# Optimization experiments

Hardware: AMD Instinct MI355X
Metric: run time of the kernel (lower is better)

Reference implementation:

```python
import jax, jax.numpy as jnp
import numpy as np

N = 16384
K = 16

def _w(k, shape):
    return jax.random.normal(k, shape, jnp.float32) * 0.05

def setup_inputs() -> dict:
    key = jax.random.key(0)
    ks = jax.random.split(key, 20)
    return {
        "img_feat": jax.random.normal(ks[0], (1, 32, N), jnp.float32),
        "cloud": jax.random.uniform(ks[1], (1, N, 3), jnp.float32),
        "conv1_w": _w(ks[2], (64, 32)),   "conv1_b": _w(ks[3], (64,)),
        "conv2_w": _w(ks[4], (128, 64)),  "conv2_b": _w(ks[5], (128,)),
        "psconv1_w": _w(ks[6], (256, 128)), "psconv1_b": _w(ks[7], (256,)),
        "psconv2_w": _w(ks[8], (128, 256)), "psconv2_b": _w(ks[9], (128,)),
        "pconv1_w": _w(ks[10], (64, 3)),  "pconv1_b": _w(ks[11], (64,)),
        "pconv2_w": _w(ks[12], (128, 64)),"pconv2_b": _w(ks[13], (128,)),
        "final_w": _w(ks[14], (32, 416)), "final_b": _w(ks[15], (32,)),
        "topk": K,
    }

def reference(img_feat, cloud, conv1_w, conv1_b, conv2_w, conv2_b,
              psconv1_w, psconv1_b, psconv2_w, psconv2_b,
              pconv1_w, pconv1_b, pconv2_w, pconv2_b,
              final_w, final_b, topk):
    lrelu = lambda x: jax.nn.leaky_relu(x, 0.01)
    pts = cloud[0]            # [N,3]  (module assumes bs=1)
    imf = img_feat[0].T       # [N,32]
    # point MLP: pconv1 -> lrelu -> pconv2 (Conv1d kernel=1 == per-point linear)
    cf = lrelu(pts @ pconv1_w.T + pconv1_b) @ pconv2_w.T + pconv2_b  # [N,128]
    # KNN: k smallest euclidean distances (self included)
    sq = jnp.sum(pts * pts, axis=-1)                 # [N]
    d2 = sq[:, None] + sq[None, :] - 2.0 * (pts @ pts.T)  # [N,N]
    _, idx = jax.lax.top_k(-d2, topk)                # [N,K]
    nb_pts = pts[idx]                                # [N,K,3]
    dist = jnp.sqrt(jnp.maximum(jnp.sum((pts[:, None, :] - nb_pts) ** 2, -1), 1e-12))
    wgt = jax.nn.softmax(-dist, axis=1)              # [N,K]
    nb_img = imf[idx]                                # [N,K,32]
    nb_cf = cf[idx]                                  # [N,K,128]
    sf = lrelu(nb_img @ conv1_w.T + conv1_b) @ conv2_w.T + conv2_b         # [N,K,128]
    sfp = lrelu(nb_cf @ psconv1_w.T + psconv1_b) @ psconv2_w.T + psconv2_b # [N,K,128]
    sf = jnp.max(sf * wgt[:, :, None], axis=1)       # weighted max-pool -> [N,128]
    sfp = jnp.max(sfp * wgt[:, :, None], axis=1)     # [N,128]
    final = jnp.concatenate([sfp, imf, sf, cf], axis=1)  # [N,416]
    out = lrelu(final) @ final_w.T + final_b         # [N,32]
    return out.T[None]                               # [1,32,N]
```

## Files before the change

### kernel.cpp

```cpp
#include <hip/hip_runtime.h>
#include <math.h>

#define N 16384
#define KNN 16
#define G 14
#define NCELL (G * G * G)

typedef __attribute__((ext_vector_type(8))) short bf16x8;
typedef __attribute__((ext_vector_type(4))) float f32x4;
typedef unsigned short ushort_t;
typedef unsigned long long u64;

__device__ __forceinline__ float lrelu(float a) { return a > 0.f ? a : 0.01f * a; }

__device__ __forceinline__ ushort_t f2bf(float f) {
  unsigned u = __float_as_uint(f);
  u += 0x7FFF + ((u >> 16) & 1);
  return (ushort_t)(u >> 16);
}
__device__ __forceinline__ float bf2f(ushort_t h) {
  return __uint_as_float((unsigned)h << 16);
}
__device__ __forceinline__ int lanerank(u64 mask) {
  return __builtin_amdgcn_mbcnt_hi((unsigned)(mask >> 32),
         __builtin_amdgcn_mbcnt_lo((unsigned)mask, 0));
}
__device__ __forceinline__ int cellof(float x) {
  int c = (int)(x * (float)G);
  return c < 0 ? 0 : (c > G - 1 ? G - 1 : c);
}
__device__ __forceinline__ int cellid(float x, float y, float z) {
  return (cellof(z) * G + cellof(y)) * G + cellof(x);
}

#define PPB 64
__global__ __launch_bounds__(256) void prepw_kernel(
    const float* __restrict__ img, const float* __restrict__ cloud,
    const float* __restrict__ p1w, const float* __restrict__ p1b,
    const float* __restrict__ p2w, const float* __restrict__ p2b,
    const float* __restrict__ ps1w, const float* __restrict__ ps2w,
    const float* __restrict__ c1w, const float* __restrict__ c2w,
    const float* __restrict__ fw,
    float4* __restrict__ pts4, ushort_t* __restrict__ cfh,
    ushort_t* __restrict__ imfh,
    ushort_t* __restrict__ w1h, ushort_t* __restrict__ w2h,
    ushort_t* __restrict__ c1h, ushort_t* __restrict__ c2h,
    float* __restrict__ fwp2, int* __restrict__ count) {
  int t = threadIdx.x;
  if (blockIdx.x >= 256) {
    int e = (blockIdx.x - 256) * 256 + t;
    if (e < 32768) w1h[e] = f2bf(ps1w[e]);
    else if (e < 65536) w2h[e - 32768] = f2bf(ps2w[e - 32768]);
    else if (e < 67584) c1h[e - 65536] = f2bf(c1w[e - 65536]);
    else if (e < 75776) c2h[e - 67584] = f2bf(c2w[e - 67584]);
    else if (e < 89088) {
      int e2 = e - 75776;
      int j4 = e2 >> 7, r2 = e2 & 127;
      int ch = r2 >> 2, sub = r2 & 3;
      fwp2[e2] = fw[ch * 416 + j4 * 4 + sub];
    }
    return;
  }
  __shared__ alignas(16) float w2t[64 * 132];
  __shared__ alignas(16) float hs[PPB * 68];
  __shared__ alignas(16) float w1s[192];
  __shared__ alignas(16) float b1s[64];
  __shared__ alignas(16) float b2s[128];
  __shared__ float ptmp[PPB * 3];
  __shared__ float psx[PPB], psy[PPB], psz[PPB];
  int pb = blockIdx.x * PPB;

  for (int e = t; e < 128 * 64; e += 256) {
    int ch = e >> 6, k = e & 63;
    w2t[k * 132 + ch] = p2w[e];
  }
  if (t < 192) w1s[t] = p1w[t];
  if (t < 64) b1s[t] = p1b[t];
  if (t < 128) b2s[t] = p2b[t];
  if (t < PPB * 3) ptmp[t] = cloud[pb * 3 + t];
  __syncthreads();
  if (t < PPB) {
    float x = ptmp[t * 3], y = ptmp[t * 3 + 1], z = ptmp[t * 3 + 2];
    psx[t] = x; psy[t] = y; psz[t] = z;
    pts4[pb + t] = make_float4(x, y, z, x * x + y * y + z * z);
    atomicAdd(&count[cellid(x, y, z)], 1);
  }
  for (int e = t; e < 32 * PPB; e += 256) {
    int c = e >> 6, p = e & 63;
    imfh[(size_t)(pb + p) * 32 + c] = f2bf(img[(size_t)c * N + pb + p]);
  }
  __syncthreads();
  for (int e = t; e < PPB * 64; e += 256) {
    int pt_ = e >> 6, ch = e & 63;
    float a = b1s[ch] + psx[pt_] * w1s[ch * 3] + psy[pt_] * w1s[ch * 3 + 1] +
              psz[pt_] * w1s[ch * 3 + 2];
    hs[pt_ * 68 + ch] = lrelu(a);
  }
  __syncthreads();
  for (int e = t; e < PPB * 32; e += 256) {
    int pt_ = e >> 5, c4 = (e & 31) << 2;
    float4 acc = *(const float4*)&b2s[c4];
    const float* hrow = &hs[pt_ * 68];
    #pragma unroll
    for (int k = 0; k < 64; k += 4) {
      float4 h4 = *(const float4*)&hrow[k];
      float4 w0 = *(const float4*)&w2t[(k + 0) * 132 + c4];
      float4 w1_ = *(const float4*)&w2t[(k + 1) * 132 + c4];
      float4 w2_ = *(const float4*)&w2t[(k + 2) * 132 + c4];
      float4 w3 = *(const float4*)&w2t[(k + 3) * 132 + c4];
      acc.x = fmaf(h4.x, w0.x, fmaf(h4.y, w1_.x, fmaf(h4.z, w2_.x, fmaf(h4.w, w3.x, acc.x))));
      acc.y = fmaf(h4.x, w0.y, fmaf(h4.y, w1_.y, fmaf(h4.z, w2_.y, fmaf(h4.w, w3.y, acc.y))));
      acc.z = fmaf(h4.x, w0.z, fmaf(h4.y, w1_.z, fmaf(h4.z, w2_.z, fmaf(h4.w, w3.z, acc.z))));
      acc.w = fmaf(h4.x, w0.w, fmaf(h4.y, w1_.w, fmaf(h4.z, w2_.w, fmaf(h4.w, w3.w, acc.w))));
    }
    unsigned lo = (unsigned)f2bf(acc.x) | ((unsigned)f2bf(acc.y) << 16);
    unsigned hi = (unsigned)f2bf(acc.z) | ((unsigned)f2bf(acc.w) << 16);
    *(uint2*)&cfh[(size_t)(pb + pt_) * 128 + c4] = make_uint2(lo, hi);
  }
}

__global__ __launch_bounds__(256) void scan_kernel(
    const int* __restrict__ count, int* __restrict__ cellStart,
    int* __restrict__ cellofs) {
  __shared__ int part[256];
  int t = threadIdx.x;
  int local[11];
  int s = 0;
  #pragma unroll
  for (int j = 0; j < 11; ++j) {
    int idx = t * 11 + j;
    local[j] = s;
    s += (idx < NCELL) ? count[idx] : 0;
  }
  part[t] = s;
  __syncthreads();
  for (int off = 1; off < 256; off <<= 1) {
    int v = (t >= off) ? part[t - off] : 0;
    __syncthreads();
    part[t] += v;
    __syncthreads();
  }
  int base = part[t] - s;
  #pragma unroll
  for (int j = 0; j < 11; ++j) {
    int idx = t * 11 + j;
    int v = base + local[j];
    if (idx < NCELL) { cellStart[idx] = v; cellofs[idx] = v; }
  }
  if (t == 255) cellStart[NCELL] = part[255];
}

__global__ __launch_bounds__(256) void scatter_kernel(
    const float4* __restrict__ pts4, int* __restrict__ cellofs,
    float4* __restrict__ spts) {
  int p = blockIdx.x * 256 + threadIdx.x;
  float4 v = pts4[p];
  int pos = atomicAdd(&cellofs[cellid(v.x, v.y, v.z)], 1);
  spts[pos] = make_float4(v.x, v.y, v.z, __int_as_float(p));
}

#define NB_LD 136
#define S1_LD 264
#define NI_LD 40
#define H1_LD 72
__global__ __launch_bounds__(256) void ymlp_kernel(
    const ushort_t* __restrict__ cfh, const ushort_t* __restrict__ imfh,
    const ushort_t* __restrict__ w1h, const float* __restrict__ b1,
    const ushort_t* __restrict__ w2h, const float* __restrict__ b2,
    const ushort_t* __restrict__ c1h, const float* __restrict__ c1b,
    const ushort_t* __restrict__ c2h, const float* __restrict__ c2b,
    ushort_t* __restrict__ ycf, ushort_t* __restrict__ yimg) {
  __shared__ ushort_t nb[64 * NB_LD];
  __shared__ ushort_t s1[64 * S1_LD];
  int t = threadIdx.x;
  int w = t >> 6, lane = t & 63;
  int col = lane & 15, quad = lane >> 4;

  if (blockIdx.x < 256) {
    int pbase = blockIdx.x * 64;
    for (int e = t; e < 1024; e += 256) {
      int row = e >> 4, c8 = (e & 15) << 3;
      *(uint4*)&nb[row * NB_LD + c8] =
          *(const uint4*)&cfh[(size_t)(pbase + row) * 128 + c8];
    }
    __syncthreads();
    f32x4 acc1[4][4];
    #pragma unroll
    for (int tt = 0; tt < 4; ++tt)
      #pragma unroll
      for (int p = 0; p < 4; ++p) acc1[tt][p] = (f32x4){0.f, 0.f, 0.f, 0.f};
    for (int k0 = 0; k0 < 128; k0 += 32) {
      bf16x8 a[4];
      #pragma unroll
      for (int p = 0; p < 4; ++p)
        a[p] = *(const bf16x8*)&nb[(p * 16 + col) * NB_LD + k0 + quad * 8];
      #pragma unroll
      for (int tt = 0; tt < 4; ++tt) {
        int n = w * 64 + tt * 16 + col;
        bf16x8 b = *(const bf16x8*)&w1h[n * 128 + k0 + quad * 8];
        #pragma unroll
        for (int p = 0; p < 4; ++p)
          acc1[tt][p] = __builtin_amdgcn_mfma_f32_16x16x32_bf16(a[p], b, acc1[tt][p], 0, 0, 0);
      }
    }
    #pragma unroll
    for (int tt = 0; tt < 4; ++tt) {
      int n = w * 64 + tt * 16 + col;
      float bb = b1[n];
      #pragma unroll
      for (int p = 0; p < 4; ++p)
        #pragma unroll
        for (int r = 0; r < 4; ++r)
          s1[(p * 16 + quad * 4 + r) * S1_LD + n] = f2bf(lrelu(acc1[tt][p][r] + bb));
    }
    __syncthreads();
    f32x4 acc2[2][4];
    #pragma unroll
    for (int tt = 0; tt < 2; ++tt)
      #pragma unroll
      for (int p = 0; p < 4; ++p) acc2[tt][p] = (f32x4){0.f, 0.f, 0.f, 0.f};
    for (int k0 = 0; k0 < 256; k0 += 32) {
      bf16x8 a[4];
      #pragma unroll
      for (int p = 0; p < 4; ++p)
        a[p] = *(const bf16x8*)&s1[(p * 16 + col) * S1_LD + k0 + quad * 8];
      #pragma unroll
      for (int tt = 0; tt < 2; ++tt) {
        int n = w * 32 + tt * 16 + col;
        bf16x8 b = *(const bf16x8*)&w2h[n * 256 + k0 + quad * 8];
        #pragma unroll
        for (int p = 0; p < 4; ++p)
          acc2[tt][p] = __builtin_amdgcn_mfma_f32_16x16x32_bf16(a[p], b, acc2[tt][p], 0, 0, 0);
      }
    }
    #pragma unroll
    for (int tt = 0; tt < 2; ++tt) {
      int n = w * 32 + tt * 16 + col;
      float bb = b2[n];
      #pragma unroll
      for (int p = 0; p < 4; ++p)
        #pragma unroll
        for (int r = 0; r < 4; ++r)
          ycf[(size_t)(pbase + p * 16 + quad * 4 + r) * 128 + n] =
              f2bf(acc2[tt][p][r] + bb);
    }
  } else {
    int pbase = (blockIdx.x - 256) * 64;
    ushort_t* nbi = nb;
    ushort_t* h1 = s1;
    {
      int row = t >> 2, c8 = (t & 3) << 3;
      *(uint4*)&nbi[row * NI_LD + c8] =
          *(const uint4*)&imfh[(size_t)(pbase + row) * 32 + c8];
    }
    __syncthreads();
    {
      f32x4 accA[4];
      #pragma unroll
      for (int p = 0; p < 4; ++p) accA[p] = (f32x4){0.f, 0.f, 0.f, 0.f};
      int n = w * 16 + col;
      bf16x8 b = *(const bf16x8*)&c1h[n * 32 + quad * 8];
      #pragma unroll
      for (int p = 0; p < 4; ++p) {
        bf16x8 a = *(const bf16x8*)&nbi[(p * 16 + col) * NI_LD + quad * 8];
        accA[p] = __builtin_amdgcn_mfma_f32_16x16x32_bf16(a, b, accA[p], 0, 0, 0);
      }
      __syncthreads();
      float bb = c1b[n];
      #pragma unroll
      for (int p = 0; p < 4; ++p)
        #pragma unroll
        for (int r = 0; r < 4; ++r)
          h1[(p * 16 + quad * 4 + r) * H1_LD + n] = f2bf(lrelu(accA[p][r] + bb));
    }
    __syncthreads();
    f32x4 acc2[2][4];
    #pragma unroll
    for (int tt = 0; tt < 2; ++tt)
      #pragma unroll
      for (int p = 0; p < 4; ++p) acc2[tt][p] = (f32x4){0.f, 0.f, 0.f, 0.f};
    for (int k0 = 0; k0 < 64; k0 += 32) {
      bf16x8 a[4];
      #pragma unroll
      for (int p = 0; p < 4; ++p)
        a[p] = *(const bf16x8*)&h1[(p * 16 + col) * H1_LD + k0 + quad * 8];
      #pragma unroll
      for (int tt = 0; tt < 2; ++tt) {
        int n = w * 32 + tt * 16 + col;
        bf16x8 b = *(const bf16x8*)&c2h[n * 64 + k0 + quad * 8];
        #pragma unroll
        for (int p = 0; p < 4; ++p)
          acc2[tt][p] = __builtin_amdgcn_mfma_f32_16x16x32_bf16(a[p], b, acc2[tt][p], 0, 0, 0);
      }
    }
    #pragma unroll
    for (int tt = 0; tt < 2; ++tt) {
      int n = w * 32 + tt * 16 + col;
      float bb = c2b[n];
      #pragma unroll
      for (int p = 0; p < 4; ++p)
        #pragma unroll
        for (int r = 0; r < 4; ++r)
          yimg[(size_t)(pbase + p * 16 + quad * 4 + r) * 128 + n] =
              f2bf(acc2[tt][p][r] + bb);
    }
  }
}

__device__ __forceinline__ float tadj(float tau, float qw) {
  float a = tau - qw;
  return a + fabsf(a) * 2e-7f + 1e-35f;
}

template <bool TWO>
__device__ __forceinline__ u64 select16_impl(u64* buf, int cnt, int lane,
                                             float& tau) {
  u64 v0 = (lane < cnt) ? buf[lane] : ~0ULL;
  u64 v1 = TWO ? ((64 + lane < cnt) ? buf[64 + lane] : ~0ULL) : ~0ULL;
  unsigned k0 = (unsigned)(v0 >> 32);
  unsigned k1 = (unsigned)(v1 >> 32);
  unsigned m = 0u;
  #pragma unroll
  for (int b = 31; b >= 0; --b) {
    unsigned probe = m | (1u << b);
    int c = __popcll(__ballot(k0 < probe));
    if (TWO) c += __popcll(__ballot(k1 < probe));
    if (c < KNN) m = probe;
  }
  int c_lt = __popcll(__ballot(k0 < m));
  if (TWO) c_lt += __popcll(__ballot(k1 < m));
  int need_eq = KNN - c_lt;
  unsigned o0 = (unsigned)v0, o1 = (unsigned)v1;
  bool e0 = (k0 == m), e1 = TWO ? (k1 == m) : false;
  int ne = __popcll(__ballot(e0));
  if (TWO) ne += __popcll(__ballot(e1));
  unsigned m2 = 0xFFFFFFFFu;
  if (ne != need_eq) {
    m2 = 0u;
    #pragma unroll
    for (int b = 13; b >= 0; --b) {
      unsigned probe = m2 | (1u << b);
      int c = __popcll(__ballot(e0 && (o0 < probe)));
      if (TWO) c += __popcll(__ballot(e1 && (o1 < probe)));
      if (c < need_eq) m2 = probe;
    }
  }
  bool s0 = (k0 < m) || (e0 && (o0 <= m2));
  u64 msk0 = __ballot(s0);
  int base0 = __popcll(msk0);
  if (s0) buf[lanerank(msk0)] = v0;
  if (TWO) {
    bool s1 = (k1 < m) || (e1 && (o1 <= m2));
    u64 msk1 = __ballot(s1);
    if (s1) buf[base0 + lanerank(msk1)] = v1;
  }
  tau = __uint_as_float(m);
  if (!(tau == tau)) tau = INFINITY;
  return buf[lane & 15];
}

__device__ __forceinline__ u64 select16(u64* buf, int& cnt, int lane,
                                        float& tau) {
  u64 r = (cnt > 64) ? select16_impl<true>(buf, cnt, lane, tau)
                     : select16_impl<false>(buf, cnt, lane, tau);
  cnt = KNN;
  return r;
}

__global__ __launch_bounds__(256) void knng_kernel(
    const float4* __restrict__ pts4, const float4* __restrict__ spts,
    const int* __restrict__ cellStart,
    const ushort_t* __restrict__ ycf, const ushort_t* __restrict__ yimg,
    const ushort_t* __restrict__ cfh, const ushort_t* __restrict__ imfh,
    const float* __restrict__ fwp2, const float* __restrict__ fb,
    float* __restrict__ outT) {
  __shared__ u64 sbuf[4][128];
  __shared__ alignas(16) float feat[4][416];
  int t = threadIdx.x;
  int wv = t >> 6, lane = t & 63;
  int sblk = (blockIdx.x & 7) * 512 + (blockIdx.x >> 3);
  int sid = sblk * 4 + wv;
  u64* buf = sbuf[wv];

  float4 q = spts[sid];
  int pid = __float_as_int(q.w);
  float qw = fmaf(q.z, q.z, fmaf(q.y, q.y, q.x * q.x));
  float q2x = -2.f * q.x, q2y = -2.f * q.y, q2z = -2.f * q.z;
  int cx = cellof(q.x), cy = cellof(q.y), cz = cellof(q.z);
  float tau = INFINITY;
  u64 vres;

  for (int r = 1;; ++r) {
    int lx = max(cx - r, 0), hx = min(cx + r, G - 1);
    int ly = max(cy - r, 0), hy = min(cy + r, G - 1);
    int lz = max(cz - r, 0), hz = min(cz + r, G - 1);
    int ny = hy - ly + 1, nz = hz - lz + 1, nruns = ny * nz;
    int cnt = 0;
    float ta = tadj(tau, qw);

    for (int rb = 0; rb < nruns; rb += 64) {
      int ln = rb + lane;
      int rs = 0, rc = 0;
      if (ln < nruns) {
        int z = lz + ln / ny, y = ly + ln % ny;
        int row = (z * G + y) * G;
        rs = cellStart[row + lx];
        rc = cellStart[row + hx + 1] - rs;
      }
      int off = rc;
      #pragma unroll
      for (int d = 1; d < 64; d <<= 1) {
        int v = __shfl_up(off, d);
        if (lane >= d) off += v;
      }
      int T = __shfl(off, 63);
      off -= rc;

      for (int cb = 0; cb < T; cb += 64) {
        int rk = cb + lane;
        int j = 0;
        #pragma unroll
        for (int step = 32; step; step >>= 1) {
          int nj = j + step;
          int onj = __shfl(off, nj & 63);
          if (nj < 64 && onj <= rk) j = nj;
        }
        int src = __shfl(rs, j) + rk - __shfl(off, j);
        bool valid = rk < T;
        if (!valid) src = 0;
        float4 c = spts[src];
        float cw = fmaf(c.z, c.z, fmaf(c.y, c.y, c.x * c.x));
        float d2 = fmaf(q2x, c.x, fmaf(q2y, c.y, fmaf(q2z, c.z, cw)));
        bool pass = valid && (d2 <= ta);
        u64 mask = __ballot(pass);
        if (mask) {
          if (pass) {
            int oid = __float_as_int(c.w);
            u64 key = ((u64)__float_as_uint(fmaxf(d2 + qw, 0.f)) << 32) | (unsigned)oid;
            buf[cnt + lanerank(mask)] = key;
          }
          cnt += __popcll(mask);
          if (cnt > 64) {
            select16(buf, cnt, lane, tau);
            ta = tadj(tau, qw);
          }
        }
      }
    }
    u64 v = select16(buf, cnt, lane, tau);
    float cl = INFINITY;
    if (lx > 0)     cl = fminf(cl, q.x - (float)lx / (float)G);
    if (hx < G - 1) cl = fminf(cl, (float)(hx + 1) / (float)G - q.x);
    if (ly > 0)     cl = fminf(cl, q.y - (float)ly / (float)G);
    if (hy < G - 1) cl = fminf(cl, (float)(hy + 1) / (float)G - q.y);
    if (lz > 0)     cl = fminf(cl, q.z - (float)lz / (float)G);
    if (hz < G - 1) cl = fminf(cl, (float)(hz + 1) / (float)G - q.z);
    bool full = (lx == 0 && hx == G - 1 && ly == 0 && hy == G - 1 &&
                 lz == 0 && hz == G - 1);
    if (full || tau * 1.00002f <= cl * cl) { vres = v; break; }
  }

  int myid = (lane < KNN) ? (int)(unsigned)(vres & 0xffffffffULL) : 0;
  float mywg = 0.f;
  {
    float4 c = pts4[myid];
    float dx = q.x - c.x, dy = q.y - c.y, dz = q.z - c.z;
    float dist = sqrtf(fmaxf(dx * dx + dy * dy + dz * dz, 1e-12f));
    float md = (lane < KNN) ? dist : INFINITY;
    #pragma unroll
    for (int off = 1; off < KNN; off <<= 1) md = fminf(md, __shfl_xor(md, off));
    float e = expf(md - dist);
    float se = (lane < KNN) ? e : 0.f;
    #pragma unroll
    for (int off = 1; off < KNN; off <<= 1) se += __shfl_xor(se, off);
    mywg = e / se;
  }

  int ksub = lane >> 4, c8 = lane & 15;
  float vimf = (lane < 32) ? bf2f(imfh[(size_t)pid * 32 + lane]) : 0.f;
  unsigned vcf = *(const unsigned*)&cfh[(size_t)pid * 128 + lane * 2];

  float a0[8], a1[8];
  #pragma unroll
  for (int j = 0; j < 8; ++j) { a0[j] = -INFINITY; a1[j] = -INFINITY; }
  #pragma unroll
  for (int kk = 0; kk < 4; ++kk) {
    int k = kk * 4 + ksub;
    int id = __shfl(myid, k);
    float wg = __shfl(mywg, k);
    uint4 v = *(const uint4*)&ycf[(size_t)id * 128 + c8 * 8];
    uint4 u = *(const uint4*)&yimg[(size_t)id * 128 + c8 * 8];
    unsigned vv[4] = {v.x, v.y, v.z, v.w};
    unsigned uu[4] = {u.x, u.y, u.z, u.w};
    #pragma unroll
    for (int h = 0; h < 4; ++h) {
      a0[h * 2]     = fmaxf(a0[h * 2],     bf2f((ushort_t)(vv[h] & 0xffff)) * wg);
      a0[h * 2 + 1] = fmaxf(a0[h * 2 + 1], bf2f((ushort_t)(vv[h] >> 16)) * wg);
      a1[h * 2]     = fmaxf(a1[h * 2],     bf2f((ushort_t)(uu[h] & 0xffff)) * wg);
      a1[h * 2 + 1] = fmaxf(a1[h * 2 + 1], bf2f((ushort_t)(uu[h] >> 16)) * wg);
    }
  }
  #pragma unroll
  for (int j = 0; j < 8; ++j) {
    a0[j] = fmaxf(a0[j], __shfl_xor(a0[j], 16));
    a0[j] = fmaxf(a0[j], __shfl_xor(a0[j], 32));
    a1[j] = fmaxf(a1[j], __shfl_xor(a1[j], 16));
    a1[j] = fmaxf(a1[j], __shfl_xor(a1[j], 32));
  }
  if (lane < 16) {
    #pragma unroll
    for (int j = 0; j < 8; ++j) {
      feat[wv][c8 * 8 + j] = lrelu(a0[j]);
      feat[wv][160 + c8 * 8 + j] = lrelu(a1[j]);
    }
  }
  if (lane < 32) feat[wv][128 + lane] = lrelu(vimf);
  feat[wv][288 + lane * 2] = lrelu(bf2f((ushort_t)(vcf & 0xffff)));
  feat[wv][288 + lane * 2 + 1] = lrelu(bf2f((ushort_t)(vcf >> 16)));

  int ch = lane & 31, half = lane >> 5;
  float acc = half ? 0.f : fb[ch];
  const float* wr = fwp2 + (half * 52) * 128 + ch * 4;
  const float* fr = &feat[wv][half * 208];
  #pragma unroll 4
  for (int j4 = 0; j4 < 52; ++j4) {
    float4 w4 = *(const float4*)(wr + j4 * 128);
    float4 f4 = *(const float4*)(fr + j4 * 4);
    acc = fmaf(f4.x, w4.x, fmaf(f4.y, w4.y, fmaf(f4.z, w4.z, fmaf(f4.w, w4.w, acc))));
  }
  acc += __shfl_xor(acc, 32);
  if (lane < 32) outT[(size_t)pid * 32 + ch] = acc;
}

__global__ __launch_bounds__(256) void tran_kernel(
    const float* __restrict__ outT, float* __restrict__ out) {
  __shared__ float tile[32][129];
  int t = threadIdx.x;
  int pbase = blockIdx.x * 128;
  #pragma unroll
  for (int i = 0; i < 16; ++i) {
    int e = i * 256 + t;
    int p = e >> 5, c = e & 31;
    tile[c][p] = outT[(size_t)(pbase + p) * 32 + c];
  }
  __syncthreads();
  #pragma unroll
  for (int i = 0; i < 16; ++i) {
    int e = i * 256 + t;
    int c = e >> 7, p = e & 127;
    out[(size_t)c * N + pbase + p] = tile[c][p];
  }
}

extern "C" void kernel_launch(void* const* d_in, const int* in_sizes, int n_in,
                              void* d_out, int out_size, void* d_ws, size_t ws_size,
                              hipStream_t stream) {
  const float* img   = (const float*)d_in[0];
  const float* cloud = (const float*)d_in[1];
  const float* c1w   = (const float*)d_in[2];
  const float* c1b   = (const float*)d_in[3];
  const float* c2w   = (const float*)d_in[4];
  const float* c2b   = (const float*)d_in[5];
  const float* ps1w  = (const float*)d_in[6];
  const float* ps1b  = (const float*)d_in[7];
  const float* ps2w  = (const float*)d_in[8];
  const float* ps2b  = (const float*)d_in[9];
  const float* p1w   = (const float*)d_in[10];
  const float* p1b   = (const float*)d_in[11];
  const float* p2w   = (const float*)d_in[12];
  const float* p2b   = (const float*)d_in[13];
  const float* fw    = (const float*)d_in[14];
  const float* fb    = (const float*)d_in[15];
  float* out = (float*)d_out;

  char* ws = (char*)d_ws;
  float4*   pts4  = (float4*)(ws + 0);
  ushort_t* cfh   = (ushort_t*)(ws + 262144);
  ushort_t* imfh  = (ushort_t*)(ws + 4456448);
  ushort_t* w1h   = (ushort_t*)(ws + 7602176);
  ushort_t* w2h   = (ushort_t*)(ws + 7667712);
  ushort_t* c1h   = (ushort_t*)(ws + 7733248);
  ushort_t* c2h   = (ushort_t*)(ws + 7737344);
  ushort_t* ycf   = (ushort_t*)(ws + 7753472);
  ushort_t* yimg  = (ushort_t*)(ws + 11947776);
  float4*   spts  = (float4*)(ws + 16142080);
  int*      cellStart = (int*)(ws + 16404224);
  int*      cellofs   = (int*)(ws + 16436992);
  int*      count     = (int*)(ws + 16453376);
  float*    fwp2      = (float*)(ws + 16469760);
  float*    outT      = (float*)(ws + 16523008);

  hipMemsetAsync(count, 0, NCELL * sizeof(int), stream);
  prepw_kernel<<<604, 256, 0, stream>>>(img, cloud, p1w, p1b, p2w, p2b,
                                        ps1w, ps2w, c1w, c2w, fw,
                                        pts4, cfh, imfh, w1h, w2h, c1h, c2h,
                                        fwp2, count);
  scan_kernel<<<1, 256, 0, stream>>>(count, cellStart, cellofs);
  scatter_kernel<<<64, 256, 0, stream>>>(pts4, cellofs, spts);
  ymlp_kernel<<<512, 256, 0, stream>>>(cfh, imfh, w1h, ps1b, w2h, ps2b,
                                       c1h, c1b, c2h, c2b, ycf, yimg);
  knng_kernel<<<N / 4, 256, 0, stream>>>(pts4, spts, cellStart,
                                         ycf, yimg, cfh, imfh,
                                         fwp2, fb, outT);
  tran_kernel<<<N / 128, 256, 0, stream>>>(outT, out);
}
```

Before: 175.4 us.

## Batch KNN selection with larger buffer, radix-4 threshold search, narrower run search

The candidate buffer grows from 128 to 256 entries per wave, and the top-16 selection now runs only once more than 192 candidates collect, instead of after 64. The threshold search resolves two bits per step with three ballots, so it needs fewer dependent rounds. The binary search that maps lanes to cell runs now uses fewer steps when a pass has few runs. Smaller changes use a fast exp intrinsic and cheaper bf16 unpacking. Selecting less often means the pruning threshold tightens later, so more candidates may be inserted, and the doubled shared buffer may lower occupancy.

```diff
diff --git a/kernel.cpp b/kernel.cpp
--- a/kernel.cpp
+++ b/kernel.cpp
@@ -20,6 +20,12 @@
 }
 __device__ __forceinline__ float bf2f(ushort_t h) {
   return __uint_as_float((unsigned)h << 16);
+}
+__device__ __forceinline__ float bflo(unsigned u) {
+  return __uint_as_float(u << 16);
+}
+__device__ __forceinline__ float bfhi(unsigned u) {
+  return __uint_as_float(u & 0xffff0000u);
 }
 __device__ __forceinline__ int lanerank(u64 mask) {
   return __builtin_amdgcn_mbcnt_hi((unsigned)(mask >> 32),
@@ -312,47 +318,63 @@
   return a + fabsf(a) * 2e-7f + 1e-35f;
 }
 
-template <bool TWO>
-__device__ __forceinline__ u64 select16_impl(u64* buf, int cnt, int lane,
-                                             float& tau) {
-  u64 v0 = (lane < cnt) ? buf[lane] : ~0ULL;
-  u64 v1 = TWO ? ((64 + lane < cnt) ? buf[64 + lane] : ~0ULL) : ~0ULL;
-  unsigned k0 = (unsigned)(v0 >> 32);
-  unsigned k1 = (unsigned)(v1 >> 32);
+template <int NS>
+__device__ __forceinline__ u64 selimpl(u64* buf, int cnt, int lane,
+                                       float& tau) {
+  u64 v[NS];
+  unsigned k[NS];
+  #pragma unroll
+  for (int s = 0; s < NS; ++s) {
+    int idx = s * 64 + lane;
+    v[s] = (idx < cnt) ? buf[idx] : ~0ULL;
+    k[s] = (unsigned)(v[s] >> 32);
+  }
   unsigned m = 0u;
   #pragma unroll
-  for (int b = 31; b >= 0; --b) {
-    unsigned probe = m | (1u << b);
-    int c = __popcll(__ballot(k0 < probe));
-    if (TWO) c += __popcll(__ballot(k1 < probe));
-    if (c < KNN) m = probe;
-  }
-  int c_lt = __popcll(__ballot(k0 < m));
-  if (TWO) c_lt += __popcll(__ballot(k1 < m));
+  for (int b = 30; b >= 0; b -= 2) {
+    unsigned p1 = m | (1u << b);
+    unsigned p2 = m | (2u << b);
+    unsigned p3 = m | (3u << b);
+    int c1 = 0, c2 = 0, c3 = 0;
+    #pragma unroll
+    for (int s = 0; s < NS; ++s) {
+      c1 += __popcll(__ballot(k[s] < p1));
+      c2 += __popcll(__ballot(k[s] < p2));
+      c3 += __popcll(__ballot(k[s] < p3));
+    }
+    if (c3 < KNN) m = p3;
+    else if (c2 < KNN) m = p2;
+    else if (c1 < KNN) m = p1;
+  }
+  int c_lt = 0, ne = 0;
+  bool e[NS];
+  #pragma unroll
+  for (int s = 0; s < NS; ++s) {
+    c_lt += __popcll(__ballot(k[s] < m));
+    e[s] = (k[s] == m);
+    ne += __popcll(__ballot(e[s]));
+  }
   int need_eq = KNN - c_lt;
-  unsigned o0 = (unsigned)v0, o1 = (unsigned)v1;
-  bool e0 = (k0 == m), e1 = TWO ? (k1 == m) : false;
-  int ne = __popcll(__ballot(e0));
-  if (TWO) ne += __popcll(__ballot(e1));
   unsigned m2 = 0xFFFFFFFFu;
   if (ne != need_eq) {
     m2 = 0u;
     #pragma unroll
     for (int b = 13; b >= 0; --b) {
       unsigned probe = m2 | (1u << b);
-      int c = __popcll(__ballot(e0 && (o0 < probe)));
-      if (TWO) c += __popcll(__ballot(e1 && (o1 < probe)));
+      int c = 0;
+      #pragma unroll
+      for (int s = 0; s < NS; ++s)
+        c += __popcll(__ballot(e[s] && ((unsigned)v[s] < probe)));
       if (c < need_eq) m2 = probe;
     }
   }
-  bool s0 = (k0 < m) || (e0 && (o0 <= m2));
-  u64 msk0 = __ballot(s0);
-  int base0 = __popcll(msk0);
-  if (s0) buf[lanerank(msk0)] = v0;
-  if (TWO) {
-    bool s1 = (k1 < m) || (e1 && (o1 <= m2));
-    u64 msk1 = __ballot(s1);
-    if (s1) buf[base0 + lanerank(msk1)] = v1;
+  int base = 0;
+  #pragma unroll
+  for (int s = 0; s < NS; ++s) {
+    bool sel = (k[s] < m) || (e[s] && ((unsigned)v[s] <= m2));
+    u64 msk = __ballot(sel);
+    if (sel) buf[base + lanerank(msk)] = v[s];
+    base += __popcll(msk);
   }
   tau = __uint_as_float(m);
   if (!(tau == tau)) tau = INFINITY;
@@ -361,8 +383,10 @@
 
 __device__ __forceinline__ u64 select16(u64* buf, int& cnt, int lane,
                                         float& tau) {
-  u64 r = (cnt > 64) ? select16_impl<true>(buf, cnt, lane, tau)
-                     : select16_impl<false>(buf, cnt, lane, tau);
+  u64 r;
+  if (cnt <= 64) r = selimpl<1>(buf, cnt, lane, tau);
+  else if (cnt <= 128) r = selimpl<2>(buf, cnt, lane, tau);
+  else r = selimpl<3>(buf, cnt, lane, tau);
   cnt = KNN;
   return r;
 }
@@ -374,7 +398,7 @@
     const ushort_t* __restrict__ cfh, const ushort_t* __restrict__ imfh,
     const float* __restrict__ fwp2, const float* __restrict__ fb,
     float* __restrict__ outT) {
-  __shared__ u64 sbuf[4][128];
+  __shared__ u64 sbuf[4][256];
   __shared__ alignas(16) float feat[4][416];
   int t = threadIdx.x;
   int wv = t >> 6, lane = t & 63;
@@ -407,6 +431,7 @@
         rs = cellStart[row + lx];
         rc = cellStart[row + hx + 1] - rs;
       }
+      int nr = nruns - rb; nr = nr > 64 ? 64 : nr;
       int off = rc;
       #pragma unroll
       for (int d = 1; d < 64; d <<= 1) {
@@ -419,11 +444,24 @@
       for (int cb = 0; cb < T; cb += 64) {
         int rk = cb + lane;
         int j = 0;
-        #pragma unroll
-        for (int step = 32; step; step >>= 1) {
-          int nj = j + step;
-          int onj = __shfl(off, nj & 63);
-          if (nj < 64 && onj <= rk) j = nj;
+        if (nr <= 16) {
+          #pragma unroll
+          for (int step = 8; step; step >>= 1) {
+            int nj = j + step;
+            if (__shfl(off, nj) <= rk) j = nj;
+          }
+        } else if (nr <= 32) {
+          #pragma unroll
+          for (int step = 16; step; step >>= 1) {
+            int nj = j + step;
+            if (__shfl(off, nj) <= rk) j = nj;
+          }
+        } else {
+          #pragma unroll
+          for (int step = 32; step; step >>= 1) {
+            int nj = j + step;
+            if (__shfl(off, nj) <= rk) j = nj;
+          }
         }
         int src = __shfl(rs, j) + rk - __shfl(off, j);
         bool valid = rk < T;
@@ -440,8 +478,9 @@
             buf[cnt + lanerank(mask)] = key;
           }
           cnt += __popcll(mask);
-          if (cnt > 64) {
-            select16(buf, cnt, lane, tau);
+          if (cnt > 192) {
+            selimpl<4>(buf, cnt, lane, tau);
+            cnt = KNN;
             ta = tadj(tau, qw);
           }
         }
@@ -469,7 +508,7 @@
     float md = (lane < KNN) ? dist : INFINITY;
     #pragma unroll
     for (int off = 1; off < KNN; off <<= 1) md = fminf(md, __shfl_xor(md, off));
-    float e = expf(md - dist);
+    float e = __expf(md - dist);
     float se = (lane < KNN) ? e : 0.f;
     #pragma unroll
     for (int off = 1; off < KNN; off <<= 1) se += __shfl_xor(se, off);
@@ -494,10 +533,10 @@
     unsigned uu[4] = {u.x, u.y, u.z, u.w};
     #pragma unroll
     for (int h = 0; h < 4; ++h) {
-      a0[h * 2]     = fmaxf(a0[h * 2],     bf2f((ushort_t)(vv[h] & 0xffff)) * wg);
-      a0[h * 2 + 1] = fmaxf(a0[h * 2 + 1], bf2f((ushort_t)(vv[h] >> 16)) * wg);
-      a1[h * 2]     = fmaxf(a1[h * 2],     bf2f((ushort_t)(uu[h] & 0xffff)) * wg);
-      a1[h * 2 + 1] = fmaxf(a1[h * 2 + 1], bf2f((ushort_t)(uu[h] >> 16)) * wg);
+      a0[h * 2]     = fmaxf(a0[h * 2],     bflo(vv[h]) * wg);
+      a0[h * 2 + 1] = fmaxf(a0[h * 2 + 1], bfhi(vv[h]) * wg);
+      a1[h * 2]     = fmaxf(a1[h * 2],     bflo(uu[h]) * wg);
+      a1[h * 2 + 1] = fmaxf(a1[h * 2 + 1], bfhi(uu[h]) * wg);
     }
   }
   #pragma unroll
@@ -515,8 +554,8 @@
     }
   }
   if (lane < 32) feat[wv][128 + lane] = lrelu(vimf);
-  feat[wv][288 + lane * 2] = lrelu(bf2f((ushort_t)(vcf & 0xffff)));
-  feat[wv][288 + lane * 2 + 1] = lrelu(bf2f((ushort_t)(vcf >> 16)));
+  feat[wv][288 + lane * 2] = lrelu(bflo(vcf));
+  feat[wv][288 + lane * 2 + 1] = lrelu(bfhi(vcf));
 
   int ch = lane & 31, half = lane >> 5;
   float acc = half ? 0.f : fb[ch];
```

Measured after the change: 179.7 us. 1.02x slower.
